# Performance work log

Measured on AMD Instinct MI355X. Metric: run time of the kernel, lower is better.

## Reference

```python
import jax, jax.numpy as jnp
import numpy as np

B, N, DIM = 4, 2048, 512
HEADS, DIM_HEAD = 8, 64
INNER = HEADS * DIM_HEAD  # 512
EPS = 1e-5
SCALE = DIM_HEAD ** -0.5


def _layernorm(x, g):
    # matches custom LayerNorm: unbiased=False var, no bias term
    mean = jnp.mean(x, axis=-1, keepdims=True)
    var = jnp.var(x, axis=-1, keepdims=True)
    return (x - mean) * jax.lax.rsqrt(var + EPS) * g


def setup_inputs() -> dict:
    key = jax.random.key(0)
    ks = jax.random.split(key, 6)
    x = jax.random.normal(ks[0], (B, N, DIM), dtype=jnp.float32)
    attn_bias = jax.random.normal(ks[1], (HEADS, N, N), dtype=jnp.float32)
    w_q = jax.random.normal(ks[2], (DIM, INNER), dtype=jnp.float32) * 0.02
    w_kv = jax.random.normal(ks[3], (DIM, 2 * DIM_HEAD), dtype=jnp.float32) * 0.02
    w_out = jax.random.normal(ks[4], (INNER, DIM), dtype=jnp.float32) * 0.02
    g_in = jnp.ones((DIM,), dtype=jnp.float32)
    g_out = jnp.ones((DIM,), dtype=jnp.float32)
    return {"x": x, "attn_bias": attn_bias, "w_q": w_q, "w_kv": w_kv,
            "w_out": w_out, "g_in": g_in, "g_out": g_out}


def reference(x, attn_bias, w_q, w_kv, w_out, g_in, g_out):
    b, n, _ = x.shape
    xn = _layernorm(x, g_in)                                  # [b, n, dim]
    q = (xn @ w_q).reshape(b, n, HEADS, DIM_HEAD)
    q = jnp.transpose(q, (0, 2, 1, 3)) * SCALE                # [b, h, n, d]
    kv = xn @ w_kv                                            # [b, n, 2d]
    k, v = jnp.split(kv, 2, axis=-1)                          # each [b, n, d] (multi-query)
    sim = jnp.einsum('bhid,bjd->bhij', q, k) + attn_bias      # [b, h, n, n]
    attn = jax.nn.softmax(sim, axis=-1)
    out = jnp.einsum('bhij,bjd->bhid', attn, v)               # [b, h, n, d]
    out = jnp.transpose(out, (0, 2, 1, 3)).reshape(b, n, INNER)
    out = out @ w_out                                         # [b, n, dim]
    return _layernorm(out, g_out)
```

## Files before the change

kernel.cpp:

```cpp
#include <hip/hip_runtime.h>
#include <hip/hip_bf16.h>

#define B_ 4
#define N_ 2048
#define DIM_ 512
#define HEADS_ 8
#define DHEAD_ 64
#define EPS_ 1e-5f
#define SCALE_ 0.125f

typedef __attribute__((ext_vector_type(8))) short short8;
typedef __attribute__((ext_vector_type(4))) float f32x4;
#define MFMA16(a, b, c) __builtin_amdgcn_mfma_f32_16x16x32_bf16(a, b, c, 0, 0, 0)

__device__ __forceinline__ float bf2f(__hip_bfloat16 v) { return __bfloat162float(v); }
__device__ __forceinline__ float us2f(unsigned short u) {
    __hip_bfloat16 h; *(unsigned short*)&h = u; return bf2f(h);
}
__device__ __forceinline__ float load_in(const void* p, size_t i, int isf32) {
    if (isf32) return ((const float*)p)[i];
    return bf2f(((const __hip_bfloat16*)p)[i]);
}

__global__ void detect_kernel(const unsigned int* __restrict__ g, int* __restrict__ flag) {
    if (threadIdx.x == 0 && blockIdx.x == 0)
        *flag = (*g == 0x3F800000u) ? 1 : 0;
}

__global__ __launch_bounds__(256) void transpose_w(const void* __restrict__ w,
                                                   __hip_bfloat16* __restrict__ wt,
                                                   int K, int N, const int* __restrict__ flag) {
    int isf32 = *flag;
    int idx = blockIdx.x * 256 + threadIdx.x;
    if (idx >= K * N) return;
    int k = idx / N, n = idx % N;
    wt[(size_t)n * K + k] = __float2bfloat16(load_in(w, idx, isf32));
}

__global__ __launch_bounds__(256) void ln1_kernel(const void* __restrict__ x,
                                                  const void* __restrict__ g,
                                                  __hip_bfloat16* __restrict__ out,
                                                  const int* __restrict__ flag) {
    int isf32 = *flag;
    int row = blockIdx.x;
    int tid = threadIdx.x;
    size_t base = (size_t)row * DIM_;
    float v0 = load_in(x, base + tid, isf32);
    float v1 = load_in(x, base + tid + 256, isf32);
    float s = v0 + v1;
    float sq = v0 * v0 + v1 * v1;
    for (int off = 32; off > 0; off >>= 1) {
        s += __shfl_xor(s, off, 64);
        sq += __shfl_xor(sq, off, 64);
    }
    __shared__ float ls[4], lq[4];
    int wid = tid >> 6;
    if ((tid & 63) == 0) { ls[wid] = s; lq[wid] = sq; }
    __syncthreads();
    s = ls[0] + ls[1] + ls[2] + ls[3];
    sq = lq[0] + lq[1] + lq[2] + lq[3];
    float mean = s * (1.0f / DIM_);
    float var = sq * (1.0f / DIM_) - mean * mean;
    float rstd = rsqrtf(var + EPS_);
    out[base + tid]       = __float2bfloat16((v0 - mean) * rstd * load_in(g, tid, isf32));
    out[base + tid + 256] = __float2bfloat16((v1 - mean) * rstd * load_in(g, tid + 256, isf32));
}

__global__ __launch_bounds__(256) void ln2_kernel(const float* __restrict__ x,
                                                  const void* __restrict__ g,
                                                  void* __restrict__ out,
                                                  const int* __restrict__ flag) {
    int isf32 = *flag;
    int row = blockIdx.x;
    int tid = threadIdx.x;
    const float* xr = x + (size_t)row * DIM_;
    float v0 = xr[tid];
    float v1 = xr[tid + 256];
    float s = v0 + v1;
    float sq = v0 * v0 + v1 * v1;
    for (int off = 32; off > 0; off >>= 1) {
        s += __shfl_xor(s, off, 64);
        sq += __shfl_xor(sq, off, 64);
    }
    __shared__ float ls[4], lq[4];
    int wid = tid >> 6;
    if ((tid & 63) == 0) { ls[wid] = s; lq[wid] = sq; }
    __syncthreads();
    s = ls[0] + ls[1] + ls[2] + ls[3];
    sq = lq[0] + lq[1] + lq[2] + lq[3];
    float mean = s * (1.0f / DIM_);
    float var = sq * (1.0f / DIM_) - mean * mean;
    float rstd = rsqrtf(var + EPS_);
    float r0 = (v0 - mean) * rstd * load_in(g, tid, isf32);
    float r1 = (v1 - mean) * rstd * load_in(g, tid + 256, isf32);
    size_t base = (size_t)row * DIM_;
    if (isf32) {
        ((float*)out)[base + tid] = r0;
        ((float*)out)[base + tid + 256] = r1;
    } else {
        ((__hip_bfloat16*)out)[base + tid] = __float2bfloat16(r0);
        ((__hip_bfloat16*)out)[base + tid + 256] = __float2bfloat16(r1);
    }
}

__global__ __launch_bounds__(256) void gemm_mfma_kv(const __hip_bfloat16* __restrict__ A,
                                                    const __hip_bfloat16* __restrict__ Bt,
                                                    __hip_bfloat16* __restrict__ Kout,
                                                    __hip_bfloat16* __restrict__ VTout,
                                                    int M, int N, int K) {
    __shared__ __align__(16) __hip_bfloat16 As[64][72];
    __shared__ __align__(16) __hip_bfloat16 Bs[64][72];
    int tid = threadIdx.x;
    int lane = tid & 63, wave = tid >> 6;
    int quad = lane >> 4, l15 = lane & 15;
    int wr = (wave & 1) * 32, wc = (wave >> 1) * 32;
    int m0 = blockIdx.y * 64, n0 = blockIdx.x * 64;
    f32x4 acc[2][2] = {};

    for (int k0 = 0; k0 < K; k0 += 64) {
        __syncthreads();
#pragma unroll
        for (int t = 0; t < 2; ++t) {
            int idx = tid + 256 * t;
            int r = idx >> 3, cc = (idx & 7) * 8;
            *(uint4*)&As[r][cc] = *(const uint4*)(A + (size_t)(m0 + r) * K + k0 + cc);
            *(uint4*)&Bs[r][cc] = *(const uint4*)(Bt + (size_t)(n0 + r) * K + k0 + cc);
        }
        __syncthreads();
#pragma unroll
        for (int ks = 0; ks < 2; ++ks) {
            short8 a0 = *(const short8*)&As[wr + l15][ks * 32 + quad * 8];
            short8 a1 = *(const short8*)&As[wr + 16 + l15][ks * 32 + quad * 8];
            short8 b0 = *(const short8*)&Bs[wc + l15][ks * 32 + quad * 8];
            short8 b1 = *(const short8*)&Bs[wc + 16 + l15][ks * 32 + quad * 8];
            acc[0][0] = MFMA16(a0, b0, acc[0][0]);
            acc[0][1] = MFMA16(a0, b1, acc[0][1]);
            acc[1][0] = MFMA16(a1, b0, acc[1][0]);
            acc[1][1] = MFMA16(a1, b1, acc[1][1]);
        }
    }
#pragma unroll
    for (int i = 0; i < 2; ++i)
#pragma unroll
        for (int j = 0; j < 2; ++j)
#pragma unroll
            for (int r = 0; r < 4; ++r) {
                int row = m0 + wr + i * 16 + quad * 4 + r;
                int col = n0 + wc + j * 16 + l15;
                float v = acc[i][j][r];
                if (col < 64)
                    Kout[(size_t)row * 64 + col] = __float2bfloat16(v);
                else
                    VTout[((size_t)((row >> 11) * 64 + (col - 64)) << 11) + (row & 2047)] = __float2bfloat16(v);
            }
}

template <int MODE>
__global__ __launch_bounds__(256) void gemm_mfma128(const __hip_bfloat16* __restrict__ A,
                                                    const __hip_bfloat16* __restrict__ Bt,
                                                    void* __restrict__ Cout,
                                                    int M, int N, int K) {
    __shared__ __align__(16) __hip_bfloat16 As[128][72];
    __shared__ __align__(16) __hip_bfloat16 Bs[128][72];
    int tid = threadIdx.x;
    int lane = tid & 63, wave = tid >> 6;
    int quad = lane >> 4, l15 = lane & 15;
    int wr = (wave & 1) * 64, wc = (wave >> 1) * 64;
    int m0 = blockIdx.y * 128, n0 = blockIdx.x * 128;
    f32x4 acc[4][4] = {};

    for (int k0 = 0; k0 < K; k0 += 64) {
        __syncthreads();
#pragma unroll
        for (int t = 0; t < 4; ++t) {
            int idx = tid + 256 * t;
            int r = idx >> 3, cc = (idx & 7) * 8;
            *(uint4*)&As[r][cc] = *(const uint4*)(A + (size_t)(m0 + r) * K + k0 + cc);
            *(uint4*)&Bs[r][cc] = *(const uint4*)(Bt + (size_t)(n0 + r) * K + k0 + cc);
        }
        __syncthreads();
#pragma unroll
        for (int ks = 0; ks < 2; ++ks) {
            short8 a[4], b[4];
#pragma unroll
            for (int i = 0; i < 4; ++i) {
                a[i] = *(const short8*)&As[wr + i * 16 + l15][ks * 32 + quad * 8];
                b[i] = *(const short8*)&Bs[wc + i * 16 + l15][ks * 32 + quad * 8];
            }
#pragma unroll
            for (int i = 0; i < 4; ++i)
#pragma unroll
                for (int j = 0; j < 4; ++j)
                    acc[i][j] = MFMA16(a[i], b[j], acc[i][j]);
        }
    }
#pragma unroll
    for (int i = 0; i < 4; ++i)
#pragma unroll
        for (int j = 0; j < 4; ++j)
#pragma unroll
            for (int r = 0; r < 4; ++r) {
                int row = m0 + wr + i * 16 + quad * 4 + r;
                int col = n0 + wc + j * 16 + l15;
                float v = acc[i][j][r];
                if (MODE == 0)
                    ((__hip_bfloat16*)Cout)[(size_t)row * N + col] = __float2bfloat16(v * SCALE_);
                else
                    ((float*)Cout)[(size_t)row * N + col] = v;
            }
}

__global__ __launch_bounds__(256) void attn_mfma(const __hip_bfloat16* __restrict__ qb,
                                                 const __hip_bfloat16* __restrict__ kb,
                                                 const __hip_bfloat16* __restrict__ vtb,
                                                 const void* __restrict__ bias,
                                                 __hip_bfloat16* __restrict__ ao,
                                                 const int* __restrict__ flag) {
    int isf32 = *flag;
    __shared__ __align__(16) __hip_bfloat16 Qs[64][72];
    __shared__ __align__(16) __hip_bfloat16 KsPs[128 * 72];
    __shared__ __align__(16) __hip_bfloat16 Vt[64][136];
    __hip_bfloat16(*Ks)[72] = (__hip_bfloat16(*)[72])KsPs;
    __hip_bfloat16(*Ps)[136] = (__hip_bfloat16(*)[136])KsPs;

    int tid = threadIdx.x;
    int lane = tid & 63, wave = tid >> 6;
    int quad = lane >> 4, l15 = lane & 15;
    int q0 = blockIdx.x * 64;
    int h = blockIdx.y, b = blockIdx.z;
    int qr = wave * 16;

#pragma unroll
    for (int t = 0; t < 2; ++t) {
        int idx = tid + 256 * t;
        int r = idx >> 3, cc = (idx & 7) * 8;
        *(uint4*)&Qs[r][cc] = *(const uint4*)(qb + (size_t)(b * N_ + q0 + r) * 512 + h * 64 + cc);
    }
    __syncthreads();
    short8 aQ0 = *(const short8*)&Qs[qr + l15][quad * 8];
    short8 aQ1 = *(const short8*)&Qs[qr + l15][32 + quad * 8];

    float m_i = -INFINITY, l_i = 0.f;
    f32x4 Oacc[4] = {};

    const char* biasp = (const char*)bias;
    const size_t brow = (size_t)h * N_ * N_ + (size_t)(q0 + qr + l15) * N_;

    for (int kb_i = 0; kb_i < N_ / 128; ++kb_i) {
        int k0 = kb_i * 128;
        __syncthreads();
#pragma unroll
        for (int t = 0; t < 4; ++t) {
            int idx = tid + 256 * t;
            int r = idx >> 3, cc = (idx & 7) * 8;
            *(uint4*)&Ks[r][cc] = *(const uint4*)(kb + (size_t)(b * N_ + k0 + r) * 64 + cc);
        }
#pragma unroll
        for (int t = 0; t < 4; ++t) {
            int idx = tid + 256 * t;
            int r = idx >> 4, cc = (idx & 15) * 8;
            *(uint4*)&Vt[r][cc] = *(const uint4*)(vtb + ((size_t)(b * 64 + r) << 11) + k0 + cc);
        }
        __syncthreads();

        float bv[8][4];
#pragma unroll
        for (int t = 0; t < 8; ++t) {
            size_t eoff = brow + k0 + t * 16 + quad * 4;
            if (isf32) {
                float4 f = *(const float4*)(biasp + eoff * 4);
                bv[t][0] = f.x; bv[t][1] = f.y; bv[t][2] = f.z; bv[t][3] = f.w;
            } else {
                ushort4 u = *(const ushort4*)(biasp + eoff * 2);
                bv[t][0] = us2f(u.x); bv[t][1] = us2f(u.y);
                bv[t][2] = us2f(u.z); bv[t][3] = us2f(u.w);
            }
        }

        f32x4 Sacc[8] = {};
#pragma unroll
        for (int t = 0; t < 8; ++t) {
            short8 k0f = *(const short8*)&Ks[t * 16 + l15][quad * 8];
            short8 k1f = *(const short8*)&Ks[t * 16 + l15][32 + quad * 8];
            Sacc[t] = MFMA16(k0f, aQ0, Sacc[t]);
            Sacc[t] = MFMA16(k1f, aQ1, Sacc[t]);
        }

        float S[8][4];
        float rm = -INFINITY;
#pragma unroll
        for (int t = 0; t < 8; ++t)
#pragma unroll
            for (int r = 0; r < 4; ++r) {
                S[t][r] = Sacc[t][r] + bv[t][r];
                rm = fmaxf(rm, S[t][r]);
            }
        rm = fmaxf(rm, __shfl_xor(rm, 16, 64));
        rm = fmaxf(rm, __shfl_xor(rm, 32, 64));
        float mnew = fmaxf(m_i, rm);
        float rs = 0.f;
#pragma unroll
        for (int t = 0; t < 8; ++t)
#pragma unroll
            for (int r = 0; r < 4; ++r) {
                S[t][r] = __expf(S[t][r] - mnew);
                rs += S[t][r];
            }
        rs += __shfl_xor(rs, 16, 64);
        rs += __shfl_xor(rs, 32, 64);
        float alpha = __expf(m_i - mnew);
        l_i = l_i * alpha + rs;
        m_i = mnew;

        float al[4];
#pragma unroll
        for (int r = 0; r < 4; ++r) al[r] = __shfl(alpha, quad * 4 + r, 64);
#pragma unroll
        for (int d = 0; d < 4; ++d)
#pragma unroll
            for (int r = 0; r < 4; ++r) Oacc[d][r] *= al[r];

        __syncthreads();
#pragma unroll
        for (int t = 0; t < 8; ++t) {
            ushort4 u;
            __hip_bfloat16 h0 = __float2bfloat16(S[t][0]);
            __hip_bfloat16 h1 = __float2bfloat16(S[t][1]);
            __hip_bfloat16 h2 = __float2bfloat16(S[t][2]);
            __hip_bfloat16 h3 = __float2bfloat16(S[t][3]);
            u.x = *(unsigned short*)&h0; u.y = *(unsigned short*)&h1;
            u.z = *(unsigned short*)&h2; u.w = *(unsigned short*)&h3;
            *(ushort4*)&Ps[qr + l15][t * 16 + quad * 4] = u;
        }

#pragma unroll
        for (int ks = 0; ks < 4; ++ks) {
            short8 aP = *(const short8*)&Ps[qr + l15][ks * 32 + quad * 8];
#pragma unroll
            for (int d = 0; d < 4; ++d) {
                short8 bV = *(const short8*)&Vt[d * 16 + l15][ks * 32 + quad * 8];
                Oacc[d] = MFMA16(aP, bV, Oacc[d]);
            }
        }
    }

    float li[4];
#pragma unroll
    for (int r = 0; r < 4; ++r) li[r] = __shfl(l_i, quad * 4 + r, 64);
#pragma unroll
    for (int d = 0; d < 4; ++d)
#pragma unroll
        for (int r = 0; r < 4; ++r) {
            float v = Oacc[d][r] / li[r];
            ao[(size_t)(b * N_ + q0 + qr + quad * 4 + r) * 512 + h * 64 + d * 16 + l15] =
                __float2bfloat16(v);
        }
}

extern "C" void kernel_launch(void* const* d_in, const int* in_sizes, int n_in,
                              void* d_out, int out_size, void* d_ws, size_t ws_size,
                              hipStream_t stream) {
    const void* x         = d_in[0];
    const void* attn_bias = d_in[1];
    const void* w_q       = d_in[2];
    const void* w_kv      = d_in[3];
    const void* w_out     = d_in[4];
    const void* g_in      = d_in[5];
    const void* g_out     = d_in[6];

    char* w = (char*)d_ws;
    __hip_bfloat16* xn   = (__hip_bfloat16*)w;
    __hip_bfloat16* qsc  = (__hip_bfloat16*)(w + (8u << 20));
    __hip_bfloat16* ao   = (__hip_bfloat16*)(w + (16u << 20));
    __hip_bfloat16* kbuf = (__hip_bfloat16*)(w + (24u << 20));
    __hip_bfloat16* vtb  = (__hip_bfloat16*)(w + (25u << 20));
    __hip_bfloat16* wqT  = (__hip_bfloat16*)(w + (26u << 20));
    __hip_bfloat16* wkvT = (__hip_bfloat16*)(w + (26u << 20) + 524288);
    __hip_bfloat16* woT  = (__hip_bfloat16*)(w + (26u << 20) + 524288 + 131072);
    int* flag            = (int*)(w + (26u << 20) + 524288 + 131072 + 524288);
    float* pj            = (float*)w;

    const int R = B_ * N_;

    hipLaunchKernelGGL(detect_kernel, dim3(1), dim3(1), 0, stream,
                       (const unsigned int*)g_in, flag);
    hipLaunchKernelGGL(transpose_w, dim3(512 * 512 / 256), dim3(256), 0, stream,
                       w_q, wqT, 512, 512, flag);
    hipLaunchKernelGGL(transpose_w, dim3(512 * 128 / 256), dim3(256), 0, stream,
                       w_kv, wkvT, 512, 128, flag);
    hipLaunchKernelGGL(transpose_w, dim3(512 * 512 / 256), dim3(256), 0, stream,
                       w_out, woT, 512, 512, flag);
    hipLaunchKernelGGL(ln1_kernel, dim3(R), dim3(256), 0, stream, x, g_in, xn, flag);
    hipLaunchKernelGGL(HIP_KERNEL_NAME(gemm_mfma128<0>), dim3(512 / 128, R / 128), dim3(256), 0, stream,
                       xn, wqT, (void*)qsc, R, 512, 512);
    hipLaunchKernelGGL(gemm_mfma_kv, dim3(128 / 64, R / 64), dim3(256), 0, stream,
                       xn, wkvT, kbuf, vtb, R, 128, 512);
    hipLaunchKernelGGL(attn_mfma, dim3(N_ / 64, HEADS_, B_), dim3(256), 0, stream,
                       qsc, kbuf, vtb, attn_bias, ao, flag);
    hipLaunchKernelGGL(HIP_KERNEL_NAME(gemm_mfma128<2>), dim3(512 / 128, R / 128), dim3(256), 0, stream,
                       ao, woT, (void*)pj, R, 512, 512);
    hipLaunchKernelGGL(ln2_kernel, dim3(R), dim3(256), 0, stream, pj, g_out, d_out, flag);
}
```

Before: 361.1 us.

## Load K/V MFMA fragments directly from global memory, drop LDS staging and barriers

The attention kernel stops staging Q, K and V^T tiles in shared memory and instead loads MFMA operand fragments straight from global memory, relying on L1/L2 caching because K/V are shared by all heads. This removes the per-iteration __syncthreads barriers and the cooperative LDS fills, leaving only a per-wave private P buffer in LDS. It also wraps the MFMA sections in s_setprio and replaces the final division with a reciprocal multiply. The trade-off is that each wave now issues redundant global loads with short-row strided access, and exposed global latency is no longer hidden by a block-wide prefetch.

```diff
diff --git a/kernel.cpp b/kernel.cpp
--- a/kernel.cpp
+++ b/kernel.cpp
@@ -217,11 +217,7 @@
                                                  __hip_bfloat16* __restrict__ ao,
                                                  const int* __restrict__ flag) {
     int isf32 = *flag;
-    __shared__ __align__(16) __hip_bfloat16 Qs[64][72];
-    __shared__ __align__(16) __hip_bfloat16 KsPs[128 * 72];
-    __shared__ __align__(16) __hip_bfloat16 Vt[64][136];
-    __hip_bfloat16(*Ks)[72] = (__hip_bfloat16(*)[72])KsPs;
-    __hip_bfloat16(*Ps)[136] = (__hip_bfloat16(*)[136])KsPs;
+    __shared__ __align__(16) __hip_bfloat16 Ps[64][140];
 
     int tid = threadIdx.x;
     int lane = tid & 63, wave = tid >> 6;
@@ -230,39 +226,19 @@
     int h = blockIdx.y, b = blockIdx.z;
     int qr = wave * 16;
 
-#pragma unroll
-    for (int t = 0; t < 2; ++t) {
-        int idx = tid + 256 * t;
-        int r = idx >> 3, cc = (idx & 7) * 8;
-        *(uint4*)&Qs[r][cc] = *(const uint4*)(qb + (size_t)(b * N_ + q0 + r) * 512 + h * 64 + cc);
-    }
-    __syncthreads();
-    short8 aQ0 = *(const short8*)&Qs[qr + l15][quad * 8];
-    short8 aQ1 = *(const short8*)&Qs[qr + l15][32 + quad * 8];
+    const __hip_bfloat16* qrow = qb + (size_t)(b * N_ + q0 + qr + l15) * 512 + h * 64;
+    short8 aQ0 = *(const short8*)(qrow + quad * 8);
+    short8 aQ1 = *(const short8*)(qrow + 32 + quad * 8);
 
     float m_i = -INFINITY, l_i = 0.f;
     f32x4 Oacc[4] = {};
 
     const char* biasp = (const char*)bias;
     const size_t brow = (size_t)h * N_ * N_ + (size_t)(q0 + qr + l15) * N_;
-
-    for (int kb_i = 0; kb_i < N_ / 128; ++kb_i) {
-        int k0 = kb_i * 128;
-        __syncthreads();
-#pragma unroll
-        for (int t = 0; t < 4; ++t) {
-            int idx = tid + 256 * t;
-            int r = idx >> 3, cc = (idx & 7) * 8;
-            *(uint4*)&Ks[r][cc] = *(const uint4*)(kb + (size_t)(b * N_ + k0 + r) * 64 + cc);
-        }
-#pragma unroll
-        for (int t = 0; t < 4; ++t) {
-            int idx = tid + 256 * t;
-            int r = idx >> 4, cc = (idx & 15) * 8;
-            *(uint4*)&Vt[r][cc] = *(const uint4*)(vtb + ((size_t)(b * 64 + r) << 11) + k0 + cc);
-        }
-        __syncthreads();
-
+    const __hip_bfloat16* kbase = kb + (size_t)b * N_ * 64;
+    const __hip_bfloat16* vbase = vtb + ((size_t)(b * 64) << 11);
+
+    for (int k0 = 0; k0 < N_; k0 += 128) {
         float bv[8][4];
 #pragma unroll
         for (int t = 0; t < 8; ++t) {
@@ -278,13 +254,16 @@
         }
 
         f32x4 Sacc[8] = {};
+        __builtin_amdgcn_s_setprio(1);
 #pragma unroll
         for (int t = 0; t < 8; ++t) {
-            short8 k0f = *(const short8*)&Ks[t * 16 + l15][quad * 8];
-            short8 k1f = *(const short8*)&Ks[t * 16 + l15][32 + quad * 8];
-            Sacc[t] = MFMA16(k0f, aQ0, Sacc[t]);
-            Sacc[t] = MFMA16(k1f, aQ1, Sacc[t]);
-        }
+            const __hip_bfloat16* krow = kbase + (size_t)(k0 + t * 16 + l15) * 64;
+            short8 kf0 = *(const short8*)(krow + quad * 8);
+            short8 kf1 = *(const short8*)(krow + 32 + quad * 8);
+            Sacc[t] = MFMA16(kf0, aQ0, Sacc[t]);
+            Sacc[t] = MFMA16(kf1, aQ1, Sacc[t]);
+        }
+        __builtin_amdgcn_s_setprio(0);
 
         float S[8][4];
         float rm = -INFINITY;
@@ -320,7 +299,6 @@
 #pragma unroll
             for (int r = 0; r < 4; ++r) Oacc[d][r] *= al[r];
 
-        __syncthreads();
 #pragma unroll
         for (int t = 0; t < 8; ++t) {
             ushort4 u;
@@ -333,25 +311,28 @@
             *(ushort4*)&Ps[qr + l15][t * 16 + quad * 4] = u;
         }
 
+        __builtin_amdgcn_s_setprio(1);
 #pragma unroll
         for (int ks = 0; ks < 4; ++ks) {
             short8 aP = *(const short8*)&Ps[qr + l15][ks * 32 + quad * 8];
 #pragma unroll
             for (int d = 0; d < 4; ++d) {
-                short8 bV = *(const short8*)&Vt[d * 16 + l15][ks * 32 + quad * 8];
+                const __hip_bfloat16* vrow = vbase + ((size_t)(d * 16 + l15) << 11) + k0;
+                short8 bV = *(const short8*)(vrow + ks * 32 + quad * 8);
                 Oacc[d] = MFMA16(aP, bV, Oacc[d]);
             }
         }
+        __builtin_amdgcn_s_setprio(0);
     }
 
     float li[4];
 #pragma unroll
-    for (int r = 0; r < 4; ++r) li[r] = __shfl(l_i, quad * 4 + r, 64);
+    for (int r = 0; r < 4; ++r) li[r] = 1.0f / __shfl(l_i, quad * 4 + r, 64);
 #pragma unroll
     for (int d = 0; d < 4; ++d)
 #pragma unroll
         for (int r = 0; r < 4; ++r) {
-            float v = Oacc[d][r] / li[r];
+            float v = Oacc[d][r] * li[r];
             ao[(size_t)(b * N_ + q0 + qr + quad * 4 + r) * 512 + h * 64 + d * 16 + l15] =
                 __float2bfloat16(v);
         }
```

New measurement: 658.0 us. +82.2%, slower.
